# Kernel tuning notes

Measured on AMD Instinct MI355X. Metric: run time of the kernel, lower is better.

The kernel has to match this reference:

```python
import jax, jax.numpy as jnp
import numpy as np

IN_CH = 256
OUT_CH = 256
STATE = 384
OUT_SEQ = 32
B_SZ = 8
SEQ = 512


def setup_inputs() -> dict:
    key = jax.random.key(0)
    ks = jax.random.split(key, 8)
    rmin, rmax, max_phase = 0.0, 1.0, 6.283
    u1 = jax.random.uniform(ks[0], (STATE,))
    u2 = jax.random.uniform(ks[1], (STATE,))
    # standard LRU stable-ring initialization
    nu_log = jnp.log(-0.5 * jnp.log(u1 * (rmax + rmin) * (rmax - rmin) + rmin ** 2))
    theta_log = jnp.log(max_phase * u2)
    lam_mod = jnp.exp(-jnp.exp(nu_log))
    gamma_log = jnp.log(jnp.sqrt(1.0 - lam_mod ** 2))
    B_re = jax.random.normal(ks[2], (STATE, IN_CH)) / np.sqrt(2 * IN_CH)
    B_im = jax.random.normal(ks[3], (STATE, IN_CH)) / np.sqrt(2 * IN_CH)
    C_re = jax.random.normal(ks[4], (OUT_CH, STATE)) / np.sqrt(STATE)
    C_im = jax.random.normal(ks[5], (OUT_CH, STATE)) / np.sqrt(STATE)
    D = jax.random.normal(ks[6], (OUT_CH, IN_CH)) / np.sqrt(IN_CH)
    x = jax.random.normal(ks[7], (B_SZ, SEQ, IN_CH))
    return dict(x=x, nu_log=nu_log, theta_log=theta_log, gamma_log=gamma_log,
                B_re=B_re, B_im=B_im, C_re=C_re, C_im=C_im, D=D)


def _lru(x, h_re, h_im, nu_log, theta_log, gamma_log, B_re, B_im, C_re, C_im, D):
    """One LRU pass over a full sequence. x: [B,S,C]. h_*: [B,N] initial complex state.
    Diagonal complex recurrence h_t = Lambda*h_{t-1} + gamma*(B x_t); y_t = Re(C h_t) + D x_t."""
    lam_mod = jnp.exp(-jnp.exp(nu_log))              # |Lambda| in (0,1)
    lre = lam_mod * jnp.cos(jnp.exp(theta_log))      # [N]
    lim = lam_mod * jnp.sin(jnp.exp(theta_log))
    gamma = jnp.exp(gamma_log)
    # input projection for whole sequence (complex, split into re/im)
    u_re = gamma * jnp.einsum('bsc,nc->bsn', x, B_re)  # [B,S,N]
    u_im = gamma * jnp.einsum('bsc,nc->bsn', x, B_im)

    def step(h, u):
        hre, him = h
        ur, ui = u
        nre = lre * hre - lim * him + ur
        nim = lre * him + lim * hre + ui
        return (nre, nim), (nre, nim)

    (h_re, h_im), (hs_re, hs_im) = jax.lax.scan(
        step, (h_re, h_im),
        (jnp.swapaxes(u_re, 0, 1), jnp.swapaxes(u_im, 0, 1)))  # scan over S
    hs_re = jnp.swapaxes(hs_re, 0, 1)  # [B,S,N]
    hs_im = jnp.swapaxes(hs_im, 0, 1)
    y = (jnp.einsum('bsn,on->bso', hs_re, C_re)
         - jnp.einsum('bsn,on->bso', hs_im, C_im)
         + jnp.einsum('bsc,oc->bso', x, D))
    return y, h_re, h_im


def reference(x, nu_log, theta_log, gamma_log, B_re, B_im, C_re, C_im, D):
    bsz = x.shape[0]
    h_re = jnp.zeros((bsz, STATE), x.dtype)   # state=None on first call -> zeros
    h_im = jnp.zeros((bsz, STATE), x.dtype)
    outs = []
    for _ in range(OUT_SEQ):
        x, h_re, h_im = _lru(x, h_re, h_im, nu_log, theta_log, gamma_log,
                             B_re, B_im, C_re, C_im, D)
        outs.append(x[:, -1:])
    return jnp.concatenate(outs, axis=-2)  # [B, OUT_SEQ, OUT_CH]
```

## Files before the change

### kernel.cpp

```cpp
#include <hip/hip_runtime.h>
#include <hip/hip_bf16.h>
#include <math.h>

typedef unsigned short u16;
typedef __attribute__((ext_vector_type(8))) short bf16x8;
typedef __attribute__((ext_vector_type(4))) float f32x4;
typedef __attribute__((ext_vector_type(16))) float f32x16;

#define IN_CH   256
#define STATE   384
#define OUT_SEQ 32
#define B_SZ    8
#define SEQ     512
#define M_ROWS  4096
#define NJ      768

#define PS_WB  (NJ*IN_CH)
#define PS_WC  (IN_CH*NJ)
#define PS_WD  (IN_CH*IN_CH)
#define PS_Z   ((size_t)M_ROWS*NJ)
#define PS_X   ((size_t)M_ROWS*IN_CH)

static constexpr size_t B_U   = 0;
static constexpr size_t B_Z   = B_U  + 8*(size_t)M_ROWS*IN_CH*4;
static constexpr size_t B_XA  = B_Z  + 3*(size_t)M_ROWS*NJ*2;
static constexpr size_t B_XB  = B_XA + 3*(size_t)M_ROWS*IN_CH*2;
static constexpr size_t B_WB  = B_XB + 3*(size_t)M_ROWS*IN_CH*2;
static constexpr size_t B_WC  = B_WB + 3*(size_t)PS_WB*2;
static constexpr size_t B_WD  = B_WC + 3*(size_t)PS_WC*2;
static constexpr size_t B_LAM = B_WD + 3*(size_t)PS_WD*2;
static constexpr size_t B_HC  = B_LAM + 2*768*4;

__device__ __forceinline__ u16 f2b(float v) {
    __hip_bfloat16 h = __float2bfloat16(v);
    return *(u16*)&h;
}
__device__ __forceinline__ float b2f(u16 u) {
    __hip_bfloat16 h = *(__hip_bfloat16*)&u;
    return __bfloat162float(h);
}
__device__ __forceinline__ void split3(float v, u16& a, u16& b, u16& c) {
    a = f2b(v);  float r1 = v  - b2f(a);
    b = f2b(r1); float r2 = r1 - b2f(b);
    c = f2b(r2);
}

__device__ __forceinline__ size_t a_idx(int row, int k, int NKC) {
    return ((size_t)(((row >> 5)*NKC + (k >> 5))*2 + ((k >> 4) & 1))*2 + ((k >> 3) & 1))*256
           + (size_t)(row & 31)*8 + (k & 7);
}

__device__ __forceinline__ void frag_decode(int r, int& t32, int& h, int& hi5,
                                            int& lo5, int& e) {
    t32 = r >> 10; int r2 = r & 1023;
    h = r2 >> 9;   int r3 = r2 & 511;
    hi5 = r3 >> 8; int r4 = r3 & 255;
    lo5 = r4 >> 3; e = r4 & 7;
}

__global__ void prep_lam_hc(const float* __restrict__ nu_log,
                            const float* __restrict__ th_log,
                            float* __restrict__ lam, float* __restrict__ lam16,
                            float* __restrict__ hc0) {
    int n = threadIdx.x;
    if (n < STATE) {
        float lm = expf(-expf(nu_log[n]));
        float th = expf(th_log[n]);
        float ar = lm * cosf(th), ai = lm * sinf(th);
        lam[2*n] = ar; lam[2*n+1] = ai;
        float pr = ar, pi = ai;
#pragma unroll
        for (int i = 0; i < 4; ++i) {
            float nr = pr*pr - pi*pi, ni = 2.f*pr*pi;
            pr = nr; pi = ni;
        }
        lam16[2*n] = pr; lam16[2*n+1] = pi;
    }
    for (int i = threadIdx.x; i < B_SZ*NJ; i += blockDim.x) hc0[i] = 0.f;
}

__global__ void prep_big(const float* __restrict__ B_re, const float* __restrict__ B_im,
                         const float* __restrict__ gamma_log,
                         const float* __restrict__ C_re, const float* __restrict__ C_im,
                         const float* __restrict__ D, const float* __restrict__ x,
                         u16* __restrict__ W, u16* __restrict__ WC, u16* __restrict__ WD,
                         u16* __restrict__ X1, u16* __restrict__ X2, u16* __restrict__ X3) {
    int idx = blockIdx.x*blockDim.x + threadIdx.x;
    if (idx < PS_WB) {
        int c32 = idx >> 13, r = idx & 8191;
        int t32,h,hi5,lo5,e; frag_decode(r, t32,h,hi5,lo5,e);
        int j = c32*32 + lo5;
        int k = t32*32 + (2*h + hi5)*8 + e;
        int n = j >> 1;
        float g = expf(gamma_log[n]);
        float v = g * ((j & 1) ? B_im[n*IN_CH + k] : B_re[n*IN_CH + k]);
        u16 a,b,cc; split3(v,a,b,cc);
        W[idx] = a; W[idx + PS_WB] = b; W[idx + 2*PS_WB] = cc;
        return;
    }
    idx -= PS_WB;
    if (idx < PS_WC) {
        int c32 = idx / 24576, r = idx % 24576;
        int t32,h,hi5,lo5,e; frag_decode(r, t32,h,hi5,lo5,e);
        int o = c32*32 + lo5;
        int j = t32*32 + (2*h + hi5)*8 + e;
        int n = j >> 1;
        float v = (j & 1) ? -C_im[o*STATE + n] : C_re[o*STATE + n];
        u16 a,b,c; split3(v,a,b,c);
        WC[idx] = a; WC[idx + PS_WC] = b; WC[idx + 2*PS_WC] = c;
        return;
    }
    idx -= PS_WC;
    if (idx < PS_WD) {
        int c32 = idx >> 13, r = idx & 8191;
        int t32,h,hi5,lo5,e; frag_decode(r, t32,h,hi5,lo5,e);
        int o = c32*32 + lo5;
        int c = t32*32 + (2*h + hi5)*8 + e;
        float v = D[o*IN_CH + c];
        u16 a,b,cc; split3(v,a,b,cc);
        WD[idx] = a; WD[idx + PS_WD] = b; WD[idx + 2*PS_WD] = cc;
        return;
    }
    idx -= PS_WD;
    {
        int row = idx >> 8, k = idx & 255;
        u16 a,b,c; split3(x[idx],a,b,c);
        size_t o = a_idx(row, k, 8);
        X1[o] = a; X2[o] = b; X3[o] = c;
    }
}

__device__ __constant__ const int cPI[6] = {0,0,1,0,1,2};
__device__ __constant__ const int cPJ[6] = {0,1,0,2,1,0};

struct G1P { const u16* A[3]; };

__global__ __launch_bounds__(512, 2)
void front_k(G1P ga, const u16* __restrict__ WBp, const u16* __restrict__ WDp,
             u16* __restrict__ Z1, u16* __restrict__ Z2, u16* __restrict__ Z3,
             float* __restrict__ P,
             const float* __restrict__ lam, const float* __restrict__ lam16,
             const float2* __restrict__ HcIn, float2* __restrict__ HcOut) {
    __shared__ __align__(16) float Ls[512*34];
    __shared__ float2 car[32][16];
    __shared__ float2 hp[32][16];
    const int tid = threadIdx.x, lane = tid & 63, w = tid >> 6;
    const int l15 = lane & 15, q = lane >> 4;
    const int hb = q >> 1, hi5q = q & 1;
    const int hi5 = lane >> 5, lo5 = lane & 31;

    if (blockIdx.x >= 192) {
        const int k0 = blockIdx.x - 192;
        const int mt = (k0 & 7)*8 + (k0 >> 3);
        const int wr = w & 1, wc = w >> 1;
        const int m32 = mt*2 + wr;
        f32x16 acc[2];
#pragma unroll
        for (int cj = 0; cj < 2; ++cj)
#pragma unroll
            for (int i = 0; i < 16; ++i) acc[cj][i] = 0.f;

        bf16x8 av[2][3][2], bv[2][2][3][2];
        auto loadA = [&](int buf, int kc) {
#pragma unroll
            for (int p = 0; p < 3; ++p)
#pragma unroll
                for (int h = 0; h < 2; ++h)
                    av[buf][p][h] = *(const bf16x8*)(ga.A[p]
                        + ((((size_t)(m32*8 + kc)*2 + h)*2 + hi5) << 8) + lo5*8);
        };
        auto loadB = [&](int buf, int kc) {
#pragma unroll
            for (int cj = 0; cj < 2; ++cj)
#pragma unroll
                for (int p = 0; p < 3; ++p)
#pragma unroll
                    for (int h = 0; h < 2; ++h)
                        bv[buf][cj][p][h] = *(const bf16x8*)(WDp + (size_t)p*PS_WD
                            + ((((size_t)((wc*2 + cj)*8 + kc)*2 + h)*2 + hi5) << 8) + lo5*8);
        };
        loadA(0, 0); loadB(0, 0);
        loadA(1, 1); loadB(1, 1);
#pragma unroll
        for (int kc = 0; kc < 8; ++kc) {
            const int cb = kc & 1;
#pragma unroll
            for (int t6 = 0; t6 < 6; ++t6)
#pragma unroll
                for (int cj = 0; cj < 2; ++cj)
#pragma unroll
                    for (int h = 0; h < 2; ++h)
                        acc[cj] = __builtin_amdgcn_mfma_f32_32x32x16_bf16(
                            av[cb][cPI[t6]][h], bv[cb][cj][cPJ[t6]][h], acc[cj], 0, 0, 0);
            if (kc + 2 < 8) { loadA(cb, kc + 2); loadB(cb, kc + 2); }
        }
#pragma unroll
        for (int cj = 0; cj < 2; ++cj)
#pragma unroll
            for (int reg = 0; reg < 16; ++reg) {
                int row = mt*64 + wr*32 + (reg & 3) + 8*(reg >> 2) + 4*hi5;
                int col = wc*64 + cj*32 + lo5;
                P[(size_t)row*IN_CH + col] = acc[cj][reg];
            }
        return;
    }

    const int b = blockIdx.x & 7, jt = blockIdx.x >> 3;

    f32x4 acc[4][2];
#pragma unroll
    for (int i = 0; i < 4; ++i)
#pragma unroll
        for (int n16 = 0; n16 < 2; ++n16) acc[i][n16] = 0.f;

    bf16x8 av[2][4][3], bv[2][2][3];
    auto loadA = [&](int buf, int kc) {
#pragma unroll
        for (int p = 0; p < 3; ++p)
#pragma unroll
            for (int i = 0; i < 4; ++i) {
                int m16 = i*8 + w;
                int row32 = b*16 + (m16 >> 1);
                int rin = ((m16 & 1) << 4) + l15;
                av[buf][i][p] = *(const bf16x8*)(ga.A[p]
                    + ((((size_t)(row32*8 + kc)*2 + hb)*2 + hi5q) << 8) + rin*8);
            }
    };
    auto loadB = [&](int buf, int kc) {
#pragma unroll
        for (int p = 0; p < 3; ++p)
#pragma unroll
            for (int n16 = 0; n16 < 2; ++n16)
                bv[buf][n16][p] = *(const bf16x8*)(WBp + (size_t)p*PS_WB
                    + ((((size_t)(jt*8 + kc)*2 + hb)*2 + hi5q) << 8) + (n16*16 + l15)*8);
    };

    loadA(0, 0); loadB(0, 0);
    loadA(1, 1); loadB(1, 1);
#pragma unroll
    for (int kc = 0; kc < 8; ++kc) {
        const int cb = kc & 1;
#pragma unroll
        for (int t6 = 0; t6 < 6; ++t6)
#pragma unroll
            for (int i = 0; i < 4; ++i)
#pragma unroll
                for (int n16 = 0; n16 < 2; ++n16)
                    acc[i][n16] = __builtin_amdgcn_mfma_f32_16x16x32_bf16(
                        av[cb][i][cPI[t6]], bv[cb][n16][cPJ[t6]], acc[i][n16], 0, 0, 0);
        if (kc + 2 < 8) { loadA(cb, kc + 2); loadB(cb, kc + 2); }
    }

#pragma unroll
    for (int i = 0; i < 4; ++i) {
        int m16 = i*8 + w;
#pragma unroll
        for (int n16 = 0; n16 < 2; ++n16)
#pragma unroll
            for (int r = 0; r < 4; ++r) {
                int s = m16*16 + q*4 + r;
                int jl = n16*16 + l15;
                Ls[s*34 + jl] = acc[i][n16][r];
            }
    }
    __syncthreads();

    {
        int st = tid & 15, ch = tid >> 4;
        int n = jt*16 + st;
        float lre = lam[2*n], lim = lam[2*n+1];
        float hr = 0.f, hm = 0.f;
#pragma unroll
        for (int t = 0; t < 16; ++t) {
            int s = ch*16 + t;
            float2 u = *(const float2*)&Ls[s*34 + 2*st];
            float nr = fmaf(lre, hr, fmaf(-lim, hm, u.x));
            float nm = fmaf(lre, hm, fmaf( lim, hr, u.y));
            hr = nr; hm = nm;
            *(float2*)&Ls[s*34 + 2*st] = make_float2(hr, hm);
        }
        car[ch][st] = make_float2(hr, hm);
    }
    __syncthreads();

    {
        int st2 = 2*w + hi5, ch2 = lane & 31;
        int n = jt*16 + st2;
        float2 e = car[ch2][st2];
        float Ar = lam16[2*n], Ai = lam16[2*n+1];
        float Br = e.x, Bi = e.y;
#pragma unroll
        for (int d = 1; d < 32; d <<= 1) {
            int src = (lane & 32) | ((lane - d) & 31);
            float pAr = __shfl(Ar, src), pAi = __shfl(Ai, src);
            float pBr = __shfl(Br, src), pBi = __shfl(Bi, src);
            if (ch2 >= d) {
                float nAr = Ar*pAr - Ai*pAi;
                float nAi = Ar*pAi + Ai*pAr;
                float nBr = fmaf(Ar, pBr, fmaf(-Ai, pBi, Br));
                float nBi = fmaf(Ar, pBi, fmaf( Ai, pBr, Bi));
                Ar = nAr; Ai = nAi; Br = nBr; Bi = nBi;
            }
        }
        float2 s0 = HcIn[(size_t)b*STATE + n];
        if (ch2 == 31) {
            float fr = fmaf(Ar, s0.x, fmaf(-Ai, s0.y, Br));
            float fi = fmaf(Ar, s0.y, fmaf( Ai, s0.x, Bi));
            HcOut[(size_t)b*STATE + n] = make_float2(fr, fi);
        }
        int srcp = (lane & 32) | ((lane - 1) & 31);
        float eAr = __shfl(Ar, srcp), eAi = __shfl(Ai, srcp);
        float eBr = __shfl(Br, srcp), eBi = __shfl(Bi, srcp);
        float sr, si;
        if (ch2 == 0) { sr = s0.x; si = s0.y; }
        else {
            sr = fmaf(eAr, s0.x, fmaf(-eAi, s0.y, eBr));
            si = fmaf(eAr, s0.y, fmaf( eAi, s0.x, eBi));
        }
        hp[ch2][st2] = make_float2(sr, si);
    }
    __syncthreads();

    {
        int st = tid & 15, ch = tid >> 4;
        int n = jt*16 + st;
        float lre = lam[2*n], lim = lam[2*n+1];
        float2 hh = hp[ch][st];
        float lpr = lre, lpi = lim;
        int j0 = jt*32 + 2*st;
#pragma unroll
        for (int t = 0; t < 16; ++t) {
            int s = ch*16 + t;
            float2 hl = *(const float2*)&Ls[s*34 + 2*st];
            float vr = fmaf(lpr, hh.x, fmaf(-lpi, hh.y, hl.x));
            float vi = fmaf(lpr, hh.y, fmaf( lpi, hh.x, hl.y));
            float nlr = lpr*lre - lpi*lim;
            float nli = lpr*lim + lpi*lre;
            lpr = nlr; lpi = nli;
            u16 a1,a2,a3, c1,c2,c3;
            split3(vr, a1,a2,a3);
            split3(vi, c1,c2,c3);
            size_t zo = a_idx(b*512 + s, j0, 24);
            ushort2 t2;
            t2.x = a1; t2.y = c1; *(ushort2*)(Z1 + zo) = t2;
            t2.x = a2; t2.y = c2; *(ushort2*)(Z2 + zo) = t2;
            t2.x = a3; t2.y = c3; *(ushort2*)(Z3 + zo) = t2;
        }
    }
}

struct G2P {
    const u16* Z[3]; const u16* WC; const float* P;
    u16* O1; u16* O2; u16* O3; float* outp; int iter;
};

__global__ __launch_bounds__(512, 2)
void gemm2_k(G2P g) {
    __shared__ __align__(16) float Lred[64*64];
    const int tid = threadIdx.x, lane = tid & 63, w = tid >> 6;
    const int kg = w >> 2, wq = w & 3;
    const int wr = wq & 1, wcq = wq >> 1;
    const int bid = blockIdx.x;
    const int b = bid & 7, mloc = (bid >> 3) & 7, n_t = bid >> 6;
    const int mtile = b*8 + mloc;
    const int m0 = mtile*64, n0 = n_t*64;
    const int hi5 = lane >> 5, lo5 = lane & 31;
    const int c32 = n_t*2 + wcq;
    const int m32 = mtile*2 + wr;
    const int cbase = kg*12;

    f32x16 accv;
#pragma unroll
    for (int i = 0; i < 16; ++i) accv[i] = 0.f;

    auto aptr = [&](int p, int c, int h) -> const u16* {
        return g.Z[p] + ((((size_t)(m32*24 + c)*2 + h)*2 + hi5) << 8) + lo5*8;
    };
    auto bptr = [&](int p, int c, int h) -> const u16* {
        return g.WC + (size_t)p*PS_WC
               + ((((size_t)(c32*24 + c)*2 + h)*2 + hi5) << 8) + lo5*8;
    };

    bf16x8 bwin[3][4][2];
    auto loadB = [&](int wnd, int tlo, int thi) {
#pragma unroll
        for (int p = 0; p < 3; ++p)
#pragma unroll
            for (int t = 0; t < 4; ++t) {
                if (t < tlo || t >= thi) continue;
#pragma unroll
                for (int h = 0; h < 2; ++h)
                    bwin[p][t][h] = *(const bf16x8*)bptr(p, cbase + wnd*4 + t, h);
            }
    };
    bf16x8 av[2][3][2];
    auto loadA = [&](int buf, int t) {
#pragma unroll
        for (int p = 0; p < 3; ++p)
#pragma unroll
            for (int h = 0; h < 2; ++h)
                av[buf][p][h] = *(const bf16x8*)aptr(p, cbase + t, h);
    };

    loadA(0, 0);
    loadB(0, 0, 4);
    loadA(1, 1);
#pragma unroll
    for (int t = 0; t < 12; ++t) {
        if ((t & 3) == 2 && t < 8) loadB((t >> 2) + 1, 0, 2);
        const int cb = t & 1;
        const int tw = t & 3;
#pragma unroll
        for (int t6 = 0; t6 < 6; ++t6)
            accv = __builtin_amdgcn_mfma_f32_32x32x16_bf16(
                av[cb][cPI[t6]][0], bwin[cPJ[t6]][tw][0],
                __builtin_amdgcn_mfma_f32_32x32x16_bf16(
                    av[cb][cPI[t6]][1], bwin[cPJ[t6]][tw][1], accv, 0, 0, 0),
                0, 0, 0);
        if ((t & 3) == 3 && t < 8) loadB((t >> 2) + 1, 2, 4);
        if (t + 2 < 12) loadA(cb, t + 2);
    }

    if (kg == 1) {
#pragma unroll
        for (int reg = 0; reg < 16; ++reg) {
            int rl = wr*32 + (reg & 3) + 8*(reg >> 2) + 4*hi5;
            int cl = wcq*32 + lo5;
            Lred[rl*64 + cl] = accv[reg];
        }
    }
    __syncthreads();
    if (kg == 0) {
#pragma unroll
        for (int reg = 0; reg < 16; ++reg) {
            int rl = wr*32 + (reg & 3) + 8*(reg >> 2) + 4*hi5;
            int cl = wcq*32 + lo5;
            int row = m0 + rl, col = n0 + cl;
            float v = accv[reg] + Lred[rl*64 + cl] + g.P[(size_t)row*IN_CH + col];
            u16 a,b,c; split3(v, a,b,c);
            size_t o = a_idx(row, col, 8);
            g.O1[o] = a; g.O2[o] = b; g.O3[o] = c;
            if ((row & (SEQ-1)) == SEQ-1)
                g.outp[(size_t)((row >> 9)*OUT_SEQ + g.iter)*IN_CH + col] = v;
        }
    }
}

extern "C" void kernel_launch(void* const* d_in, const int* in_sizes, int n_in,
                              void* d_out, int out_size, void* d_ws, size_t ws_size,
                              hipStream_t stream) {
    const float* x_in      = (const float*)d_in[0];
    const float* nu_log    = (const float*)d_in[1];
    const float* theta_log = (const float*)d_in[2];
    const float* gamma_log = (const float*)d_in[3];
    const float* B_re      = (const float*)d_in[4];
    const float* B_im      = (const float*)d_in[5];
    const float* C_re      = (const float*)d_in[6];
    const float* C_im      = (const float*)d_in[7];
    const float* D         = (const float*)d_in[8];
    float* out = (float*)d_out;

    char* ws = (char*)d_ws;
    float* P = (float*)(ws + B_U);
    u16* Z1 = (u16*)(ws + B_Z);
    u16* Z2 = Z1 + PS_Z;
    u16* Z3 = Z2 + PS_Z;
    u16* XA1 = (u16*)(ws + B_XA);
    u16* XA2 = XA1 + PS_X;
    u16* XA3 = XA2 + PS_X;
    u16* XB1 = (u16*)(ws + B_XB);
    u16* XB2 = XB1 + PS_X;
    u16* XB3 = XB2 + PS_X;
    u16* WB  = (u16*)(ws + B_WB);
    u16* WCt = (u16*)(ws + B_WC);
    u16* WDt = (u16*)(ws + B_WD);
    float* lam   = (float*)(ws + B_LAM);
    float* lam16 = lam + 768;
    float2* Hc0  = (float2*)(ws + B_HC);
    float2* Hc1  = Hc0 + (size_t)B_SZ*STATE;

    prep_lam_hc<<<1, 384, 0, stream>>>(nu_log, theta_log, lam, lam16, (float*)Hc0);
    prep_big<<<5888, 256, 0, stream>>>(B_re, B_im, gamma_log, C_re, C_im, D, x_in,
                                       WB, WCt, WDt, XA1, XA2, XA3);

    for (int it = 0; it < OUT_SEQ; ++it) {
        u16* Xc[3]; u16* Xn[3];
        if (it & 1) { Xc[0]=XB1; Xc[1]=XB2; Xc[2]=XB3; Xn[0]=XA1; Xn[1]=XA2; Xn[2]=XA3; }
        else        { Xc[0]=XA1; Xc[1]=XA2; Xc[2]=XA3; Xn[0]=XB1; Xn[1]=XB2; Xn[2]=XB3; }
        float2* Hin  = (it & 1) ? Hc1 : Hc0;
        float2* Hout = (it & 1) ? Hc0 : Hc1;

        G1P g1;
        for (int p = 0; p < 3; ++p) g1.A[p] = Xc[p];
        front_k<<<256, 512, 0, stream>>>(
            g1, WB, WDt, Z1, Z2, Z3, P, lam, lam16, Hin, Hout);

        G2P g2;
        g2.Z[0]=Z1; g2.Z[1]=Z2; g2.Z[2]=Z3;
        g2.WC = WCt; g2.P = P;
        g2.O1 = Xn[0]; g2.O2 = Xn[1]; g2.O3 = Xn[2];
        g2.outp = out; g2.iter = it;
        gemm2_k<<<256, 512, 0, stream>>>(g2);
    }
}
```

Before: 1.270 ms.

## Split gemm2 K-reduction across three wave groups instead of two

After: 1.258 ms. No clear change (-1.0%).

```diff
diff --git a/kernel.cpp b/kernel.cpp
--- a/kernel.cpp
+++ b/kernel.cpp
@@ -354,9 +354,9 @@
     u16* O1; u16* O2; u16* O3; float* outp; int iter;
 };
 
-__global__ __launch_bounds__(512, 2)
+__global__ __launch_bounds__(768, 3)
 void gemm2_k(G2P g) {
-    __shared__ __align__(16) float Lred[64*64];
+    __shared__ __align__(16) float Lred[2*4*1024];
     const int tid = threadIdx.x, lane = tid & 63, w = tid >> 6;
     const int kg = w >> 2, wq = w & 3;
     const int wr = wq & 1, wcq = wq >> 1;
@@ -367,7 +367,7 @@
     const int hi5 = lane >> 5, lo5 = lane & 31;
     const int c32 = n_t*2 + wcq;
     const int m32 = mtile*2 + wr;
-    const int cbase = kg*12;
+    const int cbase = kg*8;
 
     f32x16 accv;
 #pragma unroll
@@ -381,19 +381,7 @@
                + ((((size_t)(c32*24 + c)*2 + h)*2 + hi5) << 8) + lo5*8;
     };
 
-    bf16x8 bwin[3][4][2];
-    auto loadB = [&](int wnd, int tlo, int thi) {
-#pragma unroll
-        for (int p = 0; p < 3; ++p)
-#pragma unroll
-            for (int t = 0; t < 4; ++t) {
-                if (t < tlo || t >= thi) continue;
-#pragma unroll
-                for (int h = 0; h < 2; ++h)
-                    bwin[p][t][h] = *(const bf16x8*)bptr(p, cbase + wnd*4 + t, h);
-            }
-    };
-    bf16x8 av[2][3][2];
+    bf16x8 av[2][3][2], bv[2][3][2];
     auto loadA = [&](int buf, int t) {
 #pragma unroll
         for (int p = 0; p < 3; ++p)
@@ -401,42 +389,48 @@
             for (int h = 0; h < 2; ++h)
                 av[buf][p][h] = *(const bf16x8*)aptr(p, cbase + t, h);
     };
-
-    loadA(0, 0);
-    loadB(0, 0, 4);
-    loadA(1, 1);
-#pragma unroll
-    for (int t = 0; t < 12; ++t) {
-        if ((t & 3) == 2 && t < 8) loadB((t >> 2) + 1, 0, 2);
+    auto loadB = [&](int buf, int t) {
+#pragma unroll
+        for (int p = 0; p < 3; ++p)
+#pragma unroll
+            for (int h = 0; h < 2; ++h)
+                bv[buf][p][h] = *(const bf16x8*)bptr(p, cbase + t, h);
+    };
+
+    loadA(0, 0); loadB(0, 0);
+    loadA(1, 1); loadB(1, 1);
+#pragma unroll
+    for (int t = 0; t < 8; ++t) {
         const int cb = t & 1;
-        const int tw = t & 3;
 #pragma unroll
         for (int t6 = 0; t6 < 6; ++t6)
             accv = __builtin_amdgcn_mfma_f32_32x32x16_bf16(
-                av[cb][cPI[t6]][0], bwin[cPJ[t6]][tw][0],
+                av[cb][cPI[t6]][0], bv[cb][cPJ[t6]][0],
                 __builtin_amdgcn_mfma_f32_32x32x16_bf16(
-                    av[cb][cPI[t6]][1], bwin[cPJ[t6]][tw][1], accv, 0, 0, 0),
+                    av[cb][cPI[t6]][1], bv[cb][cPJ[t6]][1], accv, 0, 0, 0),
                 0, 0, 0);
-        if ((t & 3) == 3 && t < 8) loadB((t >> 2) + 1, 2, 4);
-        if (t + 2 < 12) loadA(cb, t + 2);
-    }
-
-    if (kg == 1) {
+        if (t + 2 < 8) { loadA(cb, t + 2); loadB(cb, t + 2); }
+    }
+
+    if (kg != 0) {
+        float* Lp = Lred + ((size_t)(kg - 1)*4 + wr*2 + wcq)*1024;
 #pragma unroll
         for (int reg = 0; reg < 16; ++reg) {
-            int rl = wr*32 + (reg & 3) + 8*(reg >> 2) + 4*hi5;
-            int cl = wcq*32 + lo5;
-            Lred[rl*64 + cl] = accv[reg];
+            int rl = (reg & 3) + 8*(reg >> 2) + 4*hi5;
+            Lp[rl*32 + lo5] = accv[reg];
         }
     }
     __syncthreads();
     if (kg == 0) {
+        const float* L1 = Lred + ((size_t)0*4 + wr*2 + wcq)*1024;
+        const float* L2 = Lred + ((size_t)1*4 + wr*2 + wcq)*1024;
 #pragma unroll
         for (int reg = 0; reg < 16; ++reg) {
-            int rl = wr*32 + (reg & 3) + 8*(reg >> 2) + 4*hi5;
-            int cl = wcq*32 + lo5;
-            int row = m0 + rl, col = n0 + cl;
-            float v = accv[reg] + Lred[rl*64 + cl] + g.P[(size_t)row*IN_CH + col];
+            int rl = (reg & 3) + 8*(reg >> 2) + 4*hi5;
+            int row = m0 + wr*32 + rl;
+            int col = n0 + wcq*32 + lo5;
+            float v = accv[reg] + L1[rl*32 + lo5] + L2[rl*32 + lo5]
+                    + g.P[(size_t)row*IN_CH + col];
             u16 a,b,c; split3(v, a,b,c);
             size_t o = a_idx(row, col, 8);
             g.O1[o] = a; g.O2[o] = b; g.O3[o] = c;
@@ -500,6 +494,6 @@
         g2.WC = WCt; g2.P = P;
         g2.O1 = Xn[0]; g2.O2 = Xn[1]; g2.O3 = Xn[2];
         g2.outp = out; g2.iter = it;
-        gemm2_k<<<256, 512, 0, stream>>>(g2);
-    }
-}
+        gemm2_k<<<256, 768, 0, stream>>>(g2);
+    }
+}
```
